# Optimization experiments

Hardware: AMD Instinct MI355X
Metric: run time of the kernel (lower is better)

The kernel has to match this reference:

```python
import jax, jax.numpy as jnp
import numpy as np

WIN_LEN = 5
RES_LEN = None


def _log_sparse_mask(Q_L, K_L, win_len=0, res_len=None):
    # Faithful port of LogSparseMask (numpy, static shapes -> constant-folded under jit)
    if res_len is None:
        L_ls = K_L - 1 - win_len
        n_reps = 1
    else:
        n_reps = int(np.ceil(K_L / res_len))
        L_ls = res_len
    l_floor = int(np.log2(L_ls))
    indxs = np.array([int(2 ** (l_floor - i)) for i in range(l_floor + 1)])
    reps_array = np.expand_dims(np.arange(n_reps, dtype='int') * L_ls, 1)
    indxs = (indxs + reps_array + win_len).flatten()
    indxs = indxs[indxs < K_L - 1]
    my_mask = np.ones(K_L, dtype='int')
    my_mask[indxs] = 0
    my_mask[:win_len + 1] = 0
    my_mask = np.concatenate([np.flip(my_mask[1:]), my_mask])
    my_mask = np.array([my_mask[K_L - i:K_L * 2 - i] for i in range(1, Q_L + 1)], dtype=bool)
    return my_mask  # [Q_L, K_L], True = masked out


def _combined_mask(L, S):
    causal = np.triu(np.ones((L, S), dtype=bool), k=1)  # TriangularCausalMask
    sparse = _log_sparse_mask(L, S, WIN_LEN, RES_LEN)
    return jnp.asarray(causal | sparse)[None, None]  # [1,1,L,S], broadcasts over B,H


def setup_inputs() -> dict:
    key = jax.random.key(0)
    k1, k2, k3 = jax.random.split(key, 3)
    B, L, H, E, D = 4, 2048, 8, 64, 64
    return {
        'queries': jax.random.normal(k1, (B, L, H, E), dtype=jnp.float32),
        'keys': jax.random.normal(k2, (B, L, H, E), dtype=jnp.float32),
        'values': jax.random.normal(k3, (B, L, H, D), dtype=jnp.float32),
    }


def reference(queries, keys, values):
    B, L, H, E = queries.shape
    S = keys.shape[1]
    scale = 1.0 / np.sqrt(E)  # self.scale is None -> 1/sqrt(E)
    # [B,H,L,S] full score matrix (eager), then causal|log-sparse masked_fill(-inf)
    scores = jnp.einsum('blhe,bshe->bhls', queries, keys)
    mask = _combined_mask(L, S)
    scores = jnp.where(mask, -jnp.inf, scale * scores)
    A = jax.nn.softmax(scores, axis=-1)  # dropout p=0.0 (eval) -> identity
    V = jnp.einsum('bhls,bshd->blhd', A, values)
    return V  # module returns (V, None); attention weights not output
```

## Files before the change

### kernel.cpp

```cpp
#include <hip/hip_runtime.h>
#include <stdint.h>


static constexpr int Bn = 4, Ln = 2048, Hn = 8, En = 64;
static constexpr int QPB = 64;
static constexpr int NT  = 512;
static constexpr int NEAR_MAX = 37;
static constexpr int SPAN = NEAR_MAX + QPB;
static constexpr int PADF = 68;
static constexpr int NNEAR = 12;
static constexpr int NFAR  = 5;
static constexpr int NDELTA = NNEAR + NFAR;

__global__ __launch_bounds__(NT) void logsparse_attn_kernel(
    const float* __restrict__ Q,
    const float* __restrict__ K,
    const float* __restrict__ V,
    float* __restrict__ O)
{
    constexpr int nearD[NNEAR] = {0,1,2,3,4,5,6,7,9,13,21,37};
    constexpr int farD[NFAR]   = {69,133,261,517,1029};

    __shared__ float Ks[SPAN * PADF];
    __shared__ float Vs[SPAN * PADF];

    const int bh = blockIdx.x & 31;
    const int l  = blockIdx.x >> 5;
    const int b  = bh >> 3;
    const int h  = bh & 7;
    const int q0 = l * QPB;

    const int tid = threadIdx.x;
    const size_t bhBase = ((size_t)b * Ln * Hn + (size_t)h) * (size_t)En;
    constexpr int ROWF = Hn * En;

    const int sub = tid & 7;
    const int qq  = tid >> 3;
    const int q   = q0 + qq;
    const int dimOff = sub * 8;
    const size_t rowQ = bhBase + (size_t)q * ROWF + dimOff;

    const float4 q0v = *(const float4*)(Q + rowQ);
    const float4 q1v = *(const float4*)(Q + rowQ + 4);

    for (int idx = tid; idx < SPAN * 16; idx += NT) {
        const int rid = idx >> 4;
        const int ch  = idx & 15;
        int g = q0 - NEAR_MAX + rid;
        if (g < 0) g = 0;
        const size_t srcOff = bhBase + (size_t)g * ROWF + ch * 4;
        const int dst = rid * PADF + ch * 4;
        *(float4*)(Ks + dst) = *(const float4*)(K + srcOff);
        *(float4*)(Vs + dst) = *(const float4*)(V + srcOff);
    }

    const float qf[8] = { q0v.x*0.125f, q0v.y*0.125f, q0v.z*0.125f, q0v.w*0.125f,
                          q1v.x*0.125f, q1v.y*0.125f, q1v.z*0.125f, q1v.w*0.125f };

    __syncthreads();

    float sc[NDELTA];
    #pragma unroll
    for (int d = 0; d < NNEAR; ++d) {
        const int del = nearD[d];
        const float* kp = Ks + (qq + NEAR_MAX - del) * PADF + dimOff;
        const float4 k0 = *(const float4*)(kp);
        const float4 k1 = *(const float4*)(kp + 4);
        float s = qf[0]*k0.x + qf[1]*k0.y + qf[2]*k0.z + qf[3]*k0.w
                + qf[4]*k1.x + qf[5]*k1.y + qf[6]*k1.z + qf[7]*k1.w;
        s += __shfl_xor(s, 1);
        s += __shfl_xor(s, 2);
        s += __shfl_xor(s, 4);
        sc[d] = (q - del < 0) ? -__builtin_inff() : s;
    }
    #pragma unroll
    for (int d = 0; d < NFAR; ++d) {
        const int del = farD[d];
        float s = -__builtin_inff();
        if (q0 + QPB - 1 >= del) {
            const int j  = q - del;
            const int jc = (j < 0) ? 0 : j;
            const float* kp = K + bhBase + (size_t)jc * ROWF + dimOff;
            const float4 k0 = *(const float4*)(kp);
            const float4 k1 = *(const float4*)(kp + 4);
            float t = qf[0]*k0.x + qf[1]*k0.y + qf[2]*k0.z + qf[3]*k0.w
                    + qf[4]*k1.x + qf[5]*k1.y + qf[6]*k1.z + qf[7]*k1.w;
            t += __shfl_xor(t, 1);
            t += __shfl_xor(t, 2);
            t += __shfl_xor(t, 4);
            s = (j < 0) ? -__builtin_inff() : t;
        }
        sc[NNEAR + d] = s;
    }

    float m = sc[0];
    #pragma unroll
    for (int d = 1; d < NDELTA; ++d) m = fmaxf(m, sc[d]);
    float sum = 0.0f;
    #pragma unroll
    for (int d = 0; d < NDELTA; ++d) {
        sc[d] = __expf(sc[d] - m);
        sum += sc[d];
    }
    const float inv = 1.0f / sum;

    float acc[8] = {0,0,0,0,0,0,0,0};
    #pragma unroll
    for (int d = 0; d < NNEAR; ++d) {
        const int del = nearD[d];
        const float* vp = Vs + (qq + NEAR_MAX - del) * PADF + dimOff;
        const float4 v0 = *(const float4*)(vp);
        const float4 v1 = *(const float4*)(vp + 4);
        const float w = sc[d];
        acc[0] = fmaf(w, v0.x, acc[0]);
        acc[1] = fmaf(w, v0.y, acc[1]);
        acc[2] = fmaf(w, v0.z, acc[2]);
        acc[3] = fmaf(w, v0.w, acc[3]);
        acc[4] = fmaf(w, v1.x, acc[4]);
        acc[5] = fmaf(w, v1.y, acc[5]);
        acc[6] = fmaf(w, v1.z, acc[6]);
        acc[7] = fmaf(w, v1.w, acc[7]);
    }
    #pragma unroll
    for (int d = 0; d < NFAR; ++d) {
        const int del = farD[d];
        if (q0 + QPB - 1 >= del) {
            const int j  = q - del;
            const int jc = (j < 0) ? 0 : j;
            const float* vp = V + bhBase + (size_t)jc * ROWF + dimOff;
            const float4 v0 = *(const float4*)(vp);
            const float4 v1 = *(const float4*)(vp + 4);
            const float w = sc[NNEAR + d];
            acc[0] = fmaf(w, v0.x, acc[0]);
            acc[1] = fmaf(w, v0.y, acc[1]);
            acc[2] = fmaf(w, v0.z, acc[2]);
            acc[3] = fmaf(w, v0.w, acc[3]);
            acc[4] = fmaf(w, v1.x, acc[4]);
            acc[5] = fmaf(w, v1.y, acc[5]);
            acc[6] = fmaf(w, v1.z, acc[6]);
            acc[7] = fmaf(w, v1.w, acc[7]);
        }
    }

    float4 o0, o1;
    o0.x = acc[0]*inv; o0.y = acc[1]*inv; o0.z = acc[2]*inv; o0.w = acc[3]*inv;
    o1.x = acc[4]*inv; o1.y = acc[5]*inv; o1.z = acc[6]*inv; o1.w = acc[7]*inv;
    *(float4*)(O + rowQ)     = o0;
    *(float4*)(O + rowQ + 4) = o1;
}

extern "C" void kernel_launch(void* const* d_in, const int* in_sizes, int n_in,
                              void* d_out, int out_size, void* d_ws, size_t ws_size,
                              hipStream_t stream) {
    const float* Q = (const float*)d_in[0];
    const float* K = (const float*)d_in[1];
    const float* V = (const float*)d_in[2];
    float* O = (float*)d_out;

    const int nblocks = Bn * Hn * (Ln / QPB);
    logsparse_attn_kernel<<<nblocks, NT, 0, stream>>>(Q, K, V, O);
}
```

Measured before the change: 100.6 us.

## Loop each block over four query chunks with register-staged double-buffered K/V tiles

Each block now handles 128 queries as four 32-query chunks with 256 threads, instead of one 64-query chunk with 512 threads. The K/V halo tile for the next chunk is loaded into registers while the current chunk computes, then written into a second shared buffer, and the next chunk's Q is prefetched. The intent is to hide global load latency behind compute. The cost is halving the grid to 512 blocks, which lowers parallelism on a large GPU, re-loading the 37-row halo for every chunk, and holding 9 staging float4 per thread, which raises register pressure.

```diff
diff --git a/kernel.cpp b/kernel.cpp
--- a/kernel.cpp
+++ b/kernel.cpp
@@ -3,14 +3,18 @@
 
 
 static constexpr int Bn = 4, Ln = 2048, Hn = 8, En = 64;
-static constexpr int QPB = 64;
-static constexpr int NT  = 512;
+static constexpr int QPC = 32;
+static constexpr int NCHUNK = 4;
+static constexpr int NT  = 256;
 static constexpr int NEAR_MAX = 37;
-static constexpr int SPAN = NEAR_MAX + QPB;
+static constexpr int SPAN = NEAR_MAX + QPC;
 static constexpr int PADF = 68;
+static constexpr int KSLOT = SPAN * 16;
+static constexpr int SLOTS = KSLOT * 2;
+static constexpr int PERT  = (SLOTS + NT - 1) / NT;
 static constexpr int NNEAR = 12;
 static constexpr int NFAR  = 5;
-static constexpr int NDELTA = NNEAR + NFAR;
+static constexpr int ND    = NNEAR + NFAR;
 
 __global__ __launch_bounds__(NT) void logsparse_attn_kernel(
     const float* __restrict__ Q,
@@ -21,14 +25,14 @@
     constexpr int nearD[NNEAR] = {0,1,2,3,4,5,6,7,9,13,21,37};
     constexpr int farD[NFAR]   = {69,133,261,517,1029};
 
-    __shared__ float Ks[SPAN * PADF];
-    __shared__ float Vs[SPAN * PADF];
-
-    const int bh = blockIdx.x & 31;
-    const int l  = blockIdx.x >> 5;
-    const int b  = bh >> 3;
-    const int h  = bh & 7;
-    const int q0 = l * QPB;
+    __shared__ float Ks[2][SPAN * PADF];
+    __shared__ float Vs[2][SPAN * PADF];
+
+    const int bh  = blockIdx.x & 31;
+    const int grp = blockIdx.x >> 5;
+    const int b   = bh >> 3;
+    const int h   = bh & 7;
+    const int qbase = grp * (QPC * NCHUNK);
 
     const int tid = threadIdx.x;
     const size_t bhBase = ((size_t)b * Ln * Hn + (size_t)h) * (size_t)En;
@@ -36,101 +40,118 @@
 
     const int sub = tid & 7;
     const int qq  = tid >> 3;
-    const int q   = q0 + qq;
     const int dimOff = sub * 8;
-    const size_t rowQ = bhBase + (size_t)q * ROWF + dimOff;
-
-    const float4 q0v = *(const float4*)(Q + rowQ);
-    const float4 q1v = *(const float4*)(Q + rowQ + 4);
-
-    for (int idx = tid; idx < SPAN * 16; idx += NT) {
-        const int rid = idx >> 4;
-        const int ch  = idx & 15;
-        int g = q0 - NEAR_MAX + rid;
-        if (g < 0) g = 0;
-        const size_t srcOff = bhBase + (size_t)g * ROWF + ch * 4;
-        const int dst = rid * PADF + ch * 4;
-        *(float4*)(Ks + dst) = *(const float4*)(K + srcOff);
-        *(float4*)(Vs + dst) = *(const float4*)(V + srcOff);
-    }
-
-    const float qf[8] = { q0v.x*0.125f, q0v.y*0.125f, q0v.z*0.125f, q0v.w*0.125f,
-                          q1v.x*0.125f, q1v.y*0.125f, q1v.z*0.125f, q1v.w*0.125f };
-
-    __syncthreads();
-
-    float sc[NDELTA];
+
+    float4 st0, st1, st2, st3, st4, st5, st6, st7, st8;
+    float4* stp[PERT] = { &st0,&st1,&st2,&st3,&st4,&st5,&st6,&st7,&st8 };
+
+    auto issueStage = [&](int qc0) {
+        #pragma unroll
+        for (int i = 0; i < PERT; ++i) {
+            int idx = tid + i * NT;
+            if (idx > SLOTS - 1) idx = SLOTS - 1;
+            const int kvi = idx >= KSLOT;
+            const int rem = idx - kvi * KSLOT;
+            const int ridi = rem >> 4, chi = rem & 15;
+            int g = qc0 - NEAR_MAX + ridi;
+            if (g < 0) g = 0;
+            const float* src = (kvi ? V : K) + bhBase + (size_t)g * ROWF + chi * 4;
+            *stp[i] = *(const float4*)src;
+        }
+    };
+    auto writeStage = [&](int bi) {
+        #pragma unroll
+        for (int i = 0; i < PERT; ++i) {
+            int idx = tid + i * NT;
+            if (idx > SLOTS - 1) idx = SLOTS - 1;
+            const int kvi = idx >= KSLOT;
+            const int rem = idx - kvi * KSLOT;
+            const int ridi = rem >> 4, chi = rem & 15;
+            float* dst = (kvi ? &Vs[bi][0] : &Ks[bi][0]) + ridi * PADF + chi * 4;
+            *(float4*)dst = *stp[i];
+        }
+    };
+
+    float4 qn0, qn1;
+    auto issueQ = [&](int qc0) {
+        const size_t rq = bhBase + (size_t)(qc0 + qq) * ROWF + dimOff;
+        qn0 = *(const float4*)(Q + rq);
+        qn1 = *(const float4*)(Q + rq + 4);
+    };
+
+    issueStage(qbase);
+    writeStage(0);
+    issueQ(qbase);
+    issueStage(qbase + QPC);
+    asm volatile("s_waitcnt lgkmcnt(0)" ::: "memory");
+    __builtin_amdgcn_sched_barrier(0);
+    __builtin_amdgcn_s_barrier();
+    __builtin_amdgcn_sched_barrier(0);
+
     #pragma unroll
-    for (int d = 0; d < NNEAR; ++d) {
-        const int del = nearD[d];
-        const float* kp = Ks + (qq + NEAR_MAX - del) * PADF + dimOff;
-        const float4 k0 = *(const float4*)(kp);
-        const float4 k1 = *(const float4*)(kp + 4);
-        float s = qf[0]*k0.x + qf[1]*k0.y + qf[2]*k0.z + qf[3]*k0.w
-                + qf[4]*k1.x + qf[5]*k1.y + qf[6]*k1.z + qf[7]*k1.w;
-        s += __shfl_xor(s, 1);
-        s += __shfl_xor(s, 2);
-        s += __shfl_xor(s, 4);
-        sc[d] = (q - del < 0) ? -__builtin_inff() : s;
-    }
-    #pragma unroll
-    for (int d = 0; d < NFAR; ++d) {
-        const int del = farD[d];
-        float s = -__builtin_inff();
-        if (q0 + QPB - 1 >= del) {
-            const int j  = q - del;
-            const int jc = (j < 0) ? 0 : j;
-            const float* kp = K + bhBase + (size_t)jc * ROWF + dimOff;
-            const float4 k0 = *(const float4*)(kp);
+    for (int c = 0; c < NCHUNK; ++c) {
+        const int qc0 = qbase + QPC * c;
+        const int q   = qc0 + qq;
+        const int bi  = c & 1;
+        const size_t rowQ = bhBase + (size_t)q * ROWF + dimOff;
+
+        const float qf[8] = { qn0.x*0.125f, qn0.y*0.125f, qn0.z*0.125f, qn0.w*0.125f,
+                              qn1.x*0.125f, qn1.y*0.125f, qn1.z*0.125f, qn1.w*0.125f };
+        if (c + 1 < NCHUNK) issueQ(qc0 + QPC);
+
+        float sc[ND];
+        #pragma unroll
+        for (int d = 0; d < NNEAR; ++d) {
+            const int del = nearD[d];
+            const float* kp = &Ks[bi][(qq + NEAR_MAX - del) * PADF + dimOff];
+            const float4 k0 = *(const float4*)kp;
             const float4 k1 = *(const float4*)(kp + 4);
-            float t = qf[0]*k0.x + qf[1]*k0.y + qf[2]*k0.z + qf[3]*k0.w
+            float s = qf[0]*k0.x + qf[1]*k0.y + qf[2]*k0.z + qf[3]*k0.w
                     + qf[4]*k1.x + qf[5]*k1.y + qf[6]*k1.z + qf[7]*k1.w;
-            t += __shfl_xor(t, 1);
-            t += __shfl_xor(t, 2);
-            t += __shfl_xor(t, 4);
-            s = (j < 0) ? -__builtin_inff() : t;
-        }
-        sc[NNEAR + d] = s;
-    }
-
-    float m = sc[0];
-    #pragma unroll
-    for (int d = 1; d < NDELTA; ++d) m = fmaxf(m, sc[d]);
-    float sum = 0.0f;
-    #pragma unroll
-    for (int d = 0; d < NDELTA; ++d) {
-        sc[d] = __expf(sc[d] - m);
-        sum += sc[d];
-    }
-    const float inv = 1.0f / sum;
-
-    float acc[8] = {0,0,0,0,0,0,0,0};
-    #pragma unroll
-    for (int d = 0; d < NNEAR; ++d) {
-        const int del = nearD[d];
-        const float* vp = Vs + (qq + NEAR_MAX - del) * PADF + dimOff;
-        const float4 v0 = *(const float4*)(vp);
-        const float4 v1 = *(const float4*)(vp + 4);
-        const float w = sc[d];
-        acc[0] = fmaf(w, v0.x, acc[0]);
-        acc[1] = fmaf(w, v0.y, acc[1]);
-        acc[2] = fmaf(w, v0.z, acc[2]);
-        acc[3] = fmaf(w, v0.w, acc[3]);
-        acc[4] = fmaf(w, v1.x, acc[4]);
-        acc[5] = fmaf(w, v1.y, acc[5]);
-        acc[6] = fmaf(w, v1.z, acc[6]);
-        acc[7] = fmaf(w, v1.w, acc[7]);
-    }
-    #pragma unroll
-    for (int d = 0; d < NFAR; ++d) {
-        const int del = farD[d];
-        if (q0 + QPB - 1 >= del) {
-            const int j  = q - del;
-            const int jc = (j < 0) ? 0 : j;
-            const float* vp = V + bhBase + (size_t)jc * ROWF + dimOff;
-            const float4 v0 = *(const float4*)(vp);
+            s += __shfl_xor(s, 1);
+            s += __shfl_xor(s, 2);
+            s += __shfl_xor(s, 4);
+            sc[d] = (q - del < 0) ? -__builtin_inff() : s;
+        }
+        #pragma unroll
+        for (int d = 0; d < NFAR; ++d) {
+            const int del = farD[d];
+            float s = -__builtin_inff();
+            if (qc0 + QPC - 1 >= del) {
+                const int j  = q - del;
+                const int jc = (j < 0) ? 0 : j;
+                const float* kp = K + bhBase + (size_t)jc * ROWF + dimOff;
+                const float4 k0 = *(const float4*)kp;
+                const float4 k1 = *(const float4*)(kp + 4);
+                float t = qf[0]*k0.x + qf[1]*k0.y + qf[2]*k0.z + qf[3]*k0.w
+                        + qf[4]*k1.x + qf[5]*k1.y + qf[6]*k1.z + qf[7]*k1.w;
+                t += __shfl_xor(t, 1);
+                t += __shfl_xor(t, 2);
+                t += __shfl_xor(t, 4);
+                s = (j < 0) ? -__builtin_inff() : t;
+            }
+            sc[NNEAR + d] = s;
+        }
+
+        float m = sc[0];
+        #pragma unroll
+        for (int d = 1; d < ND; ++d) m = fmaxf(m, sc[d]);
+        float sum = 0.0f;
+        #pragma unroll
+        for (int d = 0; d < ND; ++d) {
+            sc[d] = __expf(sc[d] - m);
+            sum += sc[d];
+        }
+        const float inv = 1.0f / sum;
+
+        float acc[8] = {0,0,0,0,0,0,0,0};
+        #pragma unroll
+        for (int d = 0; d < NNEAR; ++d) {
+            const int del = nearD[d];
+            const float* vp = &Vs[bi][(qq + NEAR_MAX - del) * PADF + dimOff];
+            const float4 v0 = *(const float4*)vp;
             const float4 v1 = *(const float4*)(vp + 4);
-            const float w = sc[NNEAR + d];
+            const float w = sc[d];
             acc[0] = fmaf(w, v0.x, acc[0]);
             acc[1] = fmaf(w, v0.y, acc[1]);
             acc[2] = fmaf(w, v0.z, acc[2]);
@@ -140,13 +161,42 @@
             acc[6] = fmaf(w, v1.z, acc[6]);
             acc[7] = fmaf(w, v1.w, acc[7]);
         }
+        #pragma unroll
+        for (int d = 0; d < NFAR; ++d) {
+            const int del = farD[d];
+            if (qc0 + QPC - 1 >= del) {
+                const int j  = q - del;
+                const int jc = (j < 0) ? 0 : j;
+                const float* vp = V + bhBase + (size_t)jc * ROWF + dimOff;
+                const float4 v0 = *(const float4*)vp;
+                const float4 v1 = *(const float4*)(vp + 4);
+                const float w = sc[NNEAR + d];
+                acc[0] = fmaf(w, v0.x, acc[0]);
+                acc[1] = fmaf(w, v0.y, acc[1]);
+                acc[2] = fmaf(w, v0.z, acc[2]);
+                acc[3] = fmaf(w, v0.w, acc[3]);
+                acc[4] = fmaf(w, v1.x, acc[4]);
+                acc[5] = fmaf(w, v1.y, acc[5]);
+                acc[6] = fmaf(w, v1.z, acc[6]);
+                acc[7] = fmaf(w, v1.w, acc[7]);
+            }
+        }
+
+        float4 o0, o1;
+        o0.x = acc[0]*inv; o0.y = acc[1]*inv; o0.z = acc[2]*inv; o0.w = acc[3]*inv;
+        o1.x = acc[4]*inv; o1.y = acc[5]*inv; o1.z = acc[6]*inv; o1.w = acc[7]*inv;
+        *(float4*)(O + rowQ)     = o0;
+        *(float4*)(O + rowQ + 4) = o1;
+
+        if (c + 1 < NCHUNK) {
+            writeStage((c + 1) & 1);
+            if (c + 2 < NCHUNK) issueStage(qc0 + 2 * QPC);
+            asm volatile("s_waitcnt lgkmcnt(0)" ::: "memory");
+            __builtin_amdgcn_sched_barrier(0);
+            __builtin_amdgcn_s_barrier();
+            __builtin_amdgcn_sched_barrier(0);
+        }
     }
-
-    float4 o0, o1;
-    o0.x = acc[0]*inv; o0.y = acc[1]*inv; o0.z = acc[2]*inv; o0.w = acc[3]*inv;
-    o1.x = acc[4]*inv; o1.y = acc[5]*inv; o1.z = acc[6]*inv; o1.w = acc[7]*inv;
-    *(float4*)(O + rowQ)     = o0;
-    *(float4*)(O + rowQ + 4) = o1;
 }
 
 extern "C" void kernel_launch(void* const* d_in, const int* in_sizes, int n_in,
@@ -157,6 +207,6 @@
     const float* V = (const float*)d_in[2];
     float* O = (float*)d_out;
 
-    const int nblocks = Bn * Hn * (Ln / QPB);
+    const int nblocks = Bn * Hn * (Ln / (QPC * NCHUNK));
     logsparse_attn_kernel<<<nblocks, NT, 0, stream>>>(Q, K, V, O);
 }
```

Result: slower. 104.0 us (+3.4%).
